# Kernel tuning notes

Measured on AMD Instinct MI355X. Metric: run time of the kernel, lower is better.

## Reference

```python
import jax, jax.numpy as jnp
import numpy as np


def setup_inputs() -> dict:
    key = jax.random.key(0)
    ks = jax.random.split(key, 8)
    B, C, W, H = 4, 256, 64, 64
    Cq = C // 8
    return {
        "input": jax.random.normal(ks[0], (B, C, W, H), dtype=jnp.float32),
        "Wf": jax.random.normal(ks[1], (Cq, C), dtype=jnp.float32) * 0.05,
        "bf": jax.random.normal(ks[2], (Cq,), dtype=jnp.float32) * 0.05,
        "Wg": jax.random.normal(ks[3], (Cq, C), dtype=jnp.float32) * 0.05,
        "bg": jax.random.normal(ks[4], (Cq,), dtype=jnp.float32) * 0.05,
        "Wh": jax.random.normal(ks[5], (C, C), dtype=jnp.float32) * 0.05,
        "bh": jax.random.normal(ks[6], (C,), dtype=jnp.float32) * 0.05,
        "gamma": jax.random.normal(ks[7], (1,), dtype=jnp.float32),
    }


def reference(input, Wf, bf, Wg, bg, Wh, bh, gamma):
    # input: [B, C, W, H]; SAGAN self-attention over N = W*H spatial tokens.
    B, C, W, H = input.shape
    N = W * H
    x = input.reshape(B, C, N)
    # 1x1 Conv1d == per-token linear projection over channels.
    f = jnp.einsum('oc,bcn->bon', Wf, x) + bf[None, :, None]  # [B, C/8, N]
    g = jnp.einsum('oc,bcn->bon', Wg, x) + bg[None, :, None]  # [B, C/8, N]
    h = jnp.einsum('oc,bcn->bon', Wh, x) + bh[None, :, None]  # [B, C,   N]
    # s = f^T g -> [B, N, N]; softmax over last dim (columns / g-tokens).
    s = jnp.einsum('bon,bom->bnm', f, g)
    attention = jax.nn.softmax(s, axis=-1)
    # out = h @ attention^T : out[b,c,m] = sum_n h[b,c,n] * attention[b,m,n]
    out = jnp.einsum('bcn,bmn->bcm', h, attention)
    out = out.reshape(B, C, W, H)
    return gamma[0] * out + input
```

## Files before the change

kernel.cpp:

```cpp
#include <hip/hip_runtime.h>

typedef _Float16 half8 __attribute__((ext_vector_type(8)));
typedef _Float16 half4 __attribute__((ext_vector_type(4)));
typedef unsigned int uintx2 __attribute__((ext_vector_type(2)));
typedef unsigned int uintx4 __attribute__((ext_vector_type(4)));
typedef float floatx16 __attribute__((ext_vector_type(16)));

#define MFMA_F16(A, B, C) __builtin_amdgcn_mfma_f32_32x32x16_f16(A, B, C, 0, 0, 0)

constexpr int Bn = 4;
constexpr int Cc = 256;
constexpr int Cq = 32;
constexpr int Nn = 4096;
constexpr float LOG2E = 1.44269504088896340736f;


__device__ inline floatx16 zero16() {
  floatx16 z;
#pragma unroll
  for (int i = 0; i < 16; ++i) z[i] = 0.f;
  return z;
}

__device__ inline unsigned int pkrtz(float a, float b) {
  return __builtin_bit_cast(unsigned int, __builtin_amdgcn_cvt_pkrtz(a, b));
}

__global__ __launch_bounds__(256) void k_wconv(
    const float* __restrict__ Wf, const float* __restrict__ Wg,
    const float* __restrict__ Wh, _Float16* __restrict__ Wfh,
    _Float16* __restrict__ Wgh, _Float16* __restrict__ Whh) {
  int e = (blockIdx.x * 256 + threadIdx.x) * 4;
  const float* src;
  _Float16* dst;
  float sc = 1.f;
  if (e < 8192) { src = Wf + e; dst = Wfh + e; sc = LOG2E; }
  else if (e < 16384) { src = Wg + (e - 8192); dst = Wgh + (e - 8192); }
  else { src = Wh + (e - 16384); dst = Whh + (e - 16384); }
  float4 v = *(const float4*)src;
  half4 o;
  o[0] = (_Float16)(v.x * sc); o[1] = (_Float16)(v.y * sc);
  o[2] = (_Float16)(v.z * sc); o[3] = (_Float16)(v.w * sc);
  *(half4*)dst = o;
}

__global__ __launch_bounds__(512) void k_qkv(
    const float* __restrict__ x,
    const _Float16* __restrict__ Wfh, const float* __restrict__ bf,
    const _Float16* __restrict__ Wgh, const float* __restrict__ bg,
    _Float16* __restrict__ Q, _Float16* __restrict__ K4,
    _Float16* __restrict__ V8) {
  __shared__ float xs[32][260];
  int tid = threadIdx.x;
  int w = tid >> 6, lane = tid & 63;
  int ml = lane & 31, h = lane >> 5;
  int b = blockIdx.x >> 7, nt = blockIdx.x & 127;
  int n0 = nt * 32;

  {
    int c = tid >> 3;
    int nl = (tid & 7) * 4;
    const float* xp = x + (size_t)b * Cc * Nn + n0 + nl;
#pragma unroll
    for (int pass = 0; pass < 4; ++pass) {
      int cc = c + pass * 64;
      float4 v = *(const float4*)(xp + (size_t)cc * Nn);
      xs[nl + 0][cc] = v.x;
      xs[nl + 1][cc] = v.y;
      xs[nl + 2][cc] = v.z;
      xs[nl + 3][cc] = v.w;
    }
  }
  __syncthreads();

  if (w < 2) {
    half8 bfr[16];
#pragma unroll
    for (int kc = 0; kc < 16; ++kc) {
      const float* xp = &xs[ml][kc * 16 + h * 8];
      half8 f;
#pragma unroll
      for (int j = 0; j < 8; ++j) f[j] = (_Float16)xp[j];
      bfr[kc] = f;
    }

    const _Float16* W = (w == 0) ? Wfh : Wgh;
    const float* bias = (w == 0) ? bf : bg;
    float bscale = (w == 0) ? LOG2E : 1.f;

    floatx16 acc = zero16();
    const _Float16* wp = W + (size_t)ml * Cc + h * 8;
#pragma unroll
    for (int kc = 0; kc < 16; ++kc) {
      half8 a = *(const half8*)(wp + kc * 16);
      acc = MFMA_F16(a, bfr[kc], acc);
    }

    if (w == 0) {
      _Float16* op = Q + ((size_t)b * Nn + n0 + ml) * Cq;
#pragma unroll
      for (int qd = 0; qd < 4; ++qd) {
        float4 bq = *(const float4*)(bias + 8 * qd + 4 * h);
        const float* bqp = (const float*)&bq;
#pragma unroll
        for (int i = 0; i < 4; ++i) {
          int crow = i + 8 * qd + 4 * h;
          op[crow] = (_Float16)(acc[4 * qd + i] + bqp[i] * bscale);
        }
      }
    } else {
#pragma unroll
      for (int qd = 0; qd < 4; ++qd) {
        float4 bq = *(const float4*)(bias + 8 * qd + 4 * h);
        const float* bqp = (const float*)&bq;
#pragma unroll
        for (int i = 0; i < 4; ++i) {
          int crow = i + 8 * qd + 4 * h;
          K4[(((size_t)b * 4 + (crow >> 3)) * Nn + n0 + ml) * 8 + (crow & 7)] =
              (_Float16)(acc[4 * qd + i] + bqp[i]);
        }
      }
    }
  }

#pragma unroll
  for (int gi = 0; gi < 2; ++gi) {
    int gidx = tid + gi * 512;
    int nbl = gidx >> 8, c = gidx & 255;
    half8 vv;
#pragma unroll
    for (int i = 0; i < 8; ++i) vv[i] = (_Float16)xs[nbl * 8 + i][c];
    *(half8*)(V8 + (((size_t)b * 512 + (n0 >> 3) + nbl) * 256 + c) * 8) = vv;
  }
}

__global__ __launch_bounds__(512) void k_rowmax(const _Float16* __restrict__ Q,
                                                const _Float16* __restrict__ K4,
                                                float* __restrict__ M) {
  __shared__ float red[8][32];
  int tid = threadIdx.x, w = tid >> 6, lane = tid & 63;
  int ml = lane & 31, h = lane >> 5;
  int b = blockIdx.x >> 7, mt = blockIdx.x & 127;
  int m0 = mt * 32;
  const _Float16* qp = Q + ((size_t)b * Nn + m0 + ml) * Cq + h * 8;
  half8 qb0 = *(const half8*)(qp);
  half8 qb1 = *(const half8*)(qp + 16);
  const _Float16* kp0 = K4 + (((size_t)b * 4 + h) * Nn + w * 512 + ml) * 8;
  const _Float16* kp1 = K4 + (((size_t)b * 4 + 2 + h) * Nn + w * 512 + ml) * 8;
  float mx = -3.0e38f;
  for (int t = 0; t < 16; ++t) {
    floatx16 s = zero16();
    half8 k0 = *(const half8*)(kp0 + (size_t)t * 32 * 8);
    half8 k1 = *(const half8*)(kp1 + (size_t)t * 32 * 8);
    s = MFMA_F16(k0, qb0, s);
    s = MFMA_F16(k1, qb1, s);
#pragma unroll
    for (int i = 0; i < 16; ++i) mx = fmaxf(mx, s[i]);
  }
  mx = fmaxf(mx, __shfl_xor(mx, 32, 64));
  if (h == 0) red[w][ml] = mx;
  __syncthreads();
  if (tid < 32) {
    float m2 = red[0][tid];
#pragma unroll
    for (int i = 1; i < 8; ++i) m2 = fmaxf(m2, red[i][tid]);
    M[(size_t)b * Nn + m0 + tid] = m2;
  }
}

__device__ inline void otree_write(float2* dst, const floatx16* o) {
#pragma unroll
  for (int cb = 0; cb < 8; ++cb)
#pragma unroll
    for (int rp = 0; rp < 8; ++rp)
      dst[(cb * 8 + rp) * 64] = make_float2(o[cb][2 * rp], o[cb][2 * rp + 1]);
}

__device__ inline void otree_add(const float2* src, floatx16* o) {
#pragma unroll
  for (int cb = 0; cb < 8; ++cb)
#pragma unroll
    for (int rp = 0; rp < 8; ++rp) {
      float2 v = src[(cb * 8 + rp) * 64];
      o[cb][2 * rp] += v.x;
      o[cb][2 * rp + 1] += v.y;
    }
}

__global__ __launch_bounds__(512, 2) void k_attn(
    const _Float16* __restrict__ Q, const _Float16* __restrict__ K4,
    const _Float16* __restrict__ V8, const float* __restrict__ M,
    const _Float16* __restrict__ Whh, const float* __restrict__ bh,
    const float* __restrict__ xin, const float* __restrict__ gamma,
    float* __restrict__ out) {
  __shared__ float Ored[4 * 8192];
  __shared__ float lred[8][32];
  int tid = threadIdx.x, w = tid >> 6, lane = tid & 63;
  int ml = lane & 31, h = lane >> 5;
  int mh = w >> 2, nw = w & 3;
  int bx = blockIdx.x;
  int mt = bx & 63, b = bx >> 6;
  int mb = mt * 64;
  int m0 = mb + mh * 32;

  const _Float16* qp = Q + ((size_t)b * Nn + m0 + ml) * Cq + h * 8;
  half8 qb0 = *(const half8*)(qp);
  half8 qb1 = *(const half8*)(qp + 16);
  float Mv = M[(size_t)b * Nn + m0 + ml];
  float g = gamma[0];
  float lacc = 0.f;

  const _Float16* k4b0 = K4 + (((size_t)b * 4 + h) * Nn + nw * 32 + ml) * 8;
  const _Float16* k4b1 = K4 + (((size_t)b * 4 + 2 + h) * Nn + nw * 32 + ml) * 8;
  const _Float16* v8b = V8 + (((size_t)b * 512 + nw * 4 + h) * 256 + ml) * 8;

  floatx16 o[8];
#pragma unroll
  for (int i = 0; i < 8; ++i) o[i] = zero16();

  half8 k0 = *(const half8*)(k4b0);
  half8 k1 = *(const half8*)(k4b1);

  for (int it = 0; it < 32; ++it) {
    floatx16 s = zero16();
    s = MFMA_F16(k0, qb0, s);
    s = MFMA_F16(k1, qb1, s);
    k0 = *(const half8*)(k4b0 + (size_t)(it + 1) * 1024);
    k1 = *(const half8*)(k4b1 + (size_t)(it + 1) * 1024);
    float p[16];
#pragma unroll
    for (int i = 0; i < 16; ++i) p[i] = __builtin_amdgcn_exp2f(s[i] - Mv);
#pragma unroll
    for (int i = 0; i < 16; ++i) lacc += p[i];
    unsigned int c0 = pkrtz(p[0], p[1]),  c1 = pkrtz(p[2], p[3]);
    unsigned int c2 = pkrtz(p[4], p[5]),  c3 = pkrtz(p[6], p[7]);
    unsigned int c4 = pkrtz(p[8], p[9]),  c5 = pkrtz(p[10], p[11]);
    unsigned int c6 = pkrtz(p[12], p[13]), c7 = pkrtz(p[14], p[15]);
    uintx2 t02 = __builtin_amdgcn_permlane32_swap(c0, c2, false, false);
    uintx2 t13 = __builtin_amdgcn_permlane32_swap(c1, c3, false, false);
    uintx2 t46 = __builtin_amdgcn_permlane32_swap(c4, c6, false, false);
    uintx2 t57 = __builtin_amdgcn_permlane32_swap(c5, c7, false, false);
    uintx4 f0v = {t02.x, t13.x, t02.y, t13.y};
    uintx4 f1v = {t46.x, t57.x, t46.y, t57.y};
    half8 pf0 = __builtin_bit_cast(half8, f0v);
    half8 pf1 = __builtin_bit_cast(half8, f1v);
    const _Float16* vp = v8b + (size_t)it * 32768;
#pragma unroll
    for (int cb = 0; cb < 8; ++cb) {
      half8 vf0 = *(const half8*)(vp + cb * 256);
      o[cb] = MFMA_F16(vf0, pf0, o[cb]);
    }
#pragma unroll
    for (int cb = 0; cb < 8; ++cb) {
      half8 vf1 = *(const half8*)(vp + 4096 + cb * 256);
      o[cb] = MFMA_F16(vf1, pf1, o[cb]);
    }
  }

  lacc += __shfl_xor(lacc, 32, 64);
  if (h == 0) lred[w][ml] = lacc;

  float2* Ored2 = (float2*)Ored;
  int lofs = h * 32 + ml;
  float2* rg0 = Ored2 + (size_t)(mh * 2) * 4096 + lofs;
  float2* rg1 = Ored2 + (size_t)(mh * 2 + 1) * 4096 + lofs;
  if (nw == 2) otree_write(rg0, o);
  if (nw == 3) otree_write(rg1, o);
  __syncthreads();
  if (nw == 0) otree_add(rg0, o);
  if (nw == 1) otree_add(rg1, o);
  __syncthreads();
  if (nw == 1) otree_write(rg1, o);
  __syncthreads();
  if (nw == 0) { otree_add(rg1, o); otree_write(rg0, o); }
  __syncthreads();

  float lv0 = lred[0][ml] + lred[1][ml] + lred[2][ml] + lred[3][ml];
  float lv1 = lred[4][ml] + lred[5][ml] + lred[6][ml] + lred[7][ml];
  float il0 = g / lv0;
  float il1 = g / lv1;
  int offs[8];
#pragma unroll
  for (int j = 0; j < 8; ++j) {
    int u = h * 8 + j;
    int rb = (u & 3) | ((u >> 3) << 2);
    int hw = (u >> 2) & 1;
    offs[j] = (rb >> 1) * 128 + hw * 64 + 2 * ml + (rb & 1);
  }
  const float* R0 = Ored;
  const float* R1 = Ored + 2 * 8192;
  int c0 = w * 32;
  const _Float16* whp = Whh + (size_t)(c0 + ml) * 256 + h * 8;
  floatx16 d0 = zero16(), d1 = zero16();
#pragma unroll
  for (int kq = 0; kq < 16; ++kq) {
    half8 a = *(const half8*)(whp + kq * 16);
    float q0[8], q1[8];
#pragma unroll
    for (int j = 0; j < 8; ++j) {
      q0[j] = R0[kq * 512 + offs[j]] * il0;
      q1[j] = R1[kq * 512 + offs[j]] * il1;
    }
    uintx4 b0v = {pkrtz(q0[0], q0[1]), pkrtz(q0[2], q0[3]),
                  pkrtz(q0[4], q0[5]), pkrtz(q0[6], q0[7])};
    uintx4 b1v = {pkrtz(q1[0], q1[1]), pkrtz(q1[2], q1[3]),
                  pkrtz(q1[4], q1[5]), pkrtz(q1[6], q1[7])};
    d0 = MFMA_F16(a, __builtin_bit_cast(half8, b0v), d0);
    d1 = MFMA_F16(a, __builtin_bit_cast(half8, b1v), d1);
  }

  size_t ob = (size_t)b * 256 * (size_t)Nn;
#pragma unroll
  for (int r = 0; r < 16; ++r) {
    int c = c0 + (r & 3) + 8 * (r >> 2) + 4 * h;
    float bias = g * bh[c];
    size_t oa0 = ob + (size_t)c * Nn + mb + ml;
    size_t oa1 = oa0 + 32;
    out[oa0] = d0[r] + bias + xin[oa0];
    out[oa1] = d1[r] + bias + xin[oa1];
  }
}

extern "C" void kernel_launch(void* const* d_in, const int* in_sizes, int n_in,
                              void* d_out, int out_size, void* d_ws,
                              size_t ws_size, hipStream_t stream) {
  const float* x = (const float*)d_in[0];
  const float* Wf = (const float*)d_in[1];
  const float* bf = (const float*)d_in[2];
  const float* Wg = (const float*)d_in[3];
  const float* bg = (const float*)d_in[4];
  const float* Wh = (const float*)d_in[5];
  const float* bh = (const float*)d_in[6];
  const float* gamma = (const float*)d_in[7];
  float* out = (float*)d_out;

  char* ws = (char*)d_ws;
  _Float16* Q  = (_Float16*)(ws);
  _Float16* K4 = (_Float16*)(ws + 1048576);
  _Float16* V8 = (_Float16*)(ws + 2097152);
  float*    M  = (float*)   (ws + 10485760);
  _Float16* Wfh = (_Float16*)(ws + 10551296);
  _Float16* Wgh = (_Float16*)(ws + 10567680);
  _Float16* Whh = (_Float16*)(ws + 10584064);

  k_wconv<<<dim3(80), dim3(256), 0, stream>>>(Wf, Wg, Wh, Wfh, Wgh, Whh);
  k_qkv<<<dim3(512), dim3(512), 0, stream>>>(x, Wfh, bf, Wgh, bg, Q, K4, V8);
  k_rowmax<<<dim3(512), dim3(512), 0, stream>>>(Q, K4, M);
  k_attn<<<dim3(256), dim3(512), 0, stream>>>(Q, K4, V8, M, Whh, bh, x, gamma, out);
}
```

Measured before the change: 151.6 us.

## Double-buffer V tiles in LDS via async global_load_lds in attention loop

Stages each 64KB V chunk into shared memory with direct global-to-LDS loads, double-buffered so the next chunk loads while the current one feeds the MFMAs. The shared buffer is reused afterwards for the output reduction. The aim is to hide global latency for V reads and to share one copy of V across the waves in a block. The cost is a block-wide barrier with full vmcnt/lgkmcnt waits every iteration, and 128KB of LDS that likely cuts occupancy from 2 blocks per CU to 1.

```diff
diff --git a/kernel.cpp b/kernel.cpp
--- a/kernel.cpp
+++ b/kernel.cpp
@@ -24,6 +24,20 @@
 
 __device__ inline unsigned int pkrtz(float a, float b) {
   return __builtin_bit_cast(unsigned int, __builtin_amdgcn_cvt_pkrtz(a, b));
+}
+
+__device__ inline void stage64k(const _Float16* __restrict__ src,
+                                _Float16* dst, int w, int lane) {
+  const char* gb = (const char*)src;
+  char* lb = (char*)dst;
+#pragma unroll
+  for (int i = 0; i < 8; ++i) {
+    int off = (w * 8 + i) * 1024;
+    __builtin_amdgcn_global_load_lds(
+        (const __attribute__((address_space(1))) unsigned int*)(gb + off + lane * 16),
+        (__attribute__((address_space(3))) unsigned int*)(lb + off),
+        16, 0, 0);
+  }
 }
 
 __global__ __launch_bounds__(256) void k_wconv(
@@ -193,8 +207,12 @@
     const _Float16* __restrict__ Whh, const float* __restrict__ bh,
     const float* __restrict__ xin, const float* __restrict__ gamma,
     float* __restrict__ out) {
-  __shared__ float Ored[4 * 8192];
+  __shared__ __align__(16) char smem[131072];
   __shared__ float lred[8][32];
+  _Float16* vbuf = (_Float16*)smem;
+  float* OredF = (float*)smem;
+  float2* Ored2 = (float2*)smem;
+
   int tid = threadIdx.x, w = tid >> 6, lane = tid & 63;
   int ml = lane & 31, h = lane >> 5;
   int mh = w >> 2, nw = w & 3;
@@ -212,21 +230,31 @@
 
   const _Float16* k4b0 = K4 + (((size_t)b * 4 + h) * Nn + nw * 32 + ml) * 8;
   const _Float16* k4b1 = K4 + (((size_t)b * 4 + 2 + h) * Nn + nw * 32 + ml) * 8;
-  const _Float16* v8b = V8 + (((size_t)b * 512 + nw * 4 + h) * 256 + ml) * 8;
+  const _Float16* vchunk = V8 + (size_t)b * 512 * 2048;
 
   floatx16 o[8];
 #pragma unroll
   for (int i = 0; i < 8; ++i) o[i] = zero16();
 
+  stage64k(vchunk, vbuf, w, lane);
   half8 k0 = *(const half8*)(k4b0);
   half8 k1 = *(const half8*)(k4b1);
+  asm volatile("s_waitcnt vmcnt(0)" ::: "memory");
+  __builtin_amdgcn_s_barrier();
+  __builtin_amdgcn_sched_barrier(0);
+
+  const _Float16* vrd = vbuf + ((nw * 4 + h) * 2048 + ml * 8);
+  int cur = 0;
 
   for (int it = 0; it < 32; ++it) {
+    if (it < 31)
+      stage64k(vchunk + (size_t)(it + 1) * 32768, vbuf + (cur ^ 1) * 32768, w, lane);
+    half8 kn0 = *(const half8*)(k4b0 + (size_t)(it + 1) * 1024);
+    half8 kn1 = *(const half8*)(k4b1 + (size_t)(it + 1) * 1024);
+
     floatx16 s = zero16();
     s = MFMA_F16(k0, qb0, s);
     s = MFMA_F16(k1, qb1, s);
-    k0 = *(const half8*)(k4b0 + (size_t)(it + 1) * 1024);
-    k1 = *(const half8*)(k4b1 + (size_t)(it + 1) * 1024);
     float p[16];
 #pragma unroll
     for (int i = 0; i < 16; ++i) p[i] = __builtin_amdgcn_exp2f(s[i] - Mv);
@@ -244,7 +272,8 @@
     uintx4 f1v = {t46.x, t57.x, t46.y, t57.y};
     half8 pf0 = __builtin_bit_cast(half8, f0v);
     half8 pf1 = __builtin_bit_cast(half8, f1v);
-    const _Float16* vp = v8b + (size_t)it * 32768;
+
+    const _Float16* vp = vrd + cur * 32768;
 #pragma unroll
     for (int cb = 0; cb < 8; ++cb) {
       half8 vf0 = *(const half8*)(vp + cb * 256);
@@ -255,12 +284,18 @@
       half8 vf1 = *(const half8*)(vp + 4096 + cb * 256);
       o[cb] = MFMA_F16(vf1, pf1, o[cb]);
     }
+
+    asm volatile("s_waitcnt lgkmcnt(0)" ::: "memory");
+    asm volatile("s_waitcnt vmcnt(0)" ::: "memory");
+    __builtin_amdgcn_s_barrier();
+    __builtin_amdgcn_sched_barrier(0);
+    cur ^= 1;
+    k0 = kn0; k1 = kn1;
   }
 
   lacc += __shfl_xor(lacc, 32, 64);
   if (h == 0) lred[w][ml] = lacc;
 
-  float2* Ored2 = (float2*)Ored;
   int lofs = h * 32 + ml;
   float2* rg0 = Ored2 + (size_t)(mh * 2) * 4096 + lofs;
   float2* rg1 = Ored2 + (size_t)(mh * 2 + 1) * 4096 + lofs;
@@ -287,10 +322,10 @@
     int hw = (u >> 2) & 1;
     offs[j] = (rb >> 1) * 128 + hw * 64 + 2 * ml + (rb & 1);
   }
-  const float* R0 = Ored;
-  const float* R1 = Ored + 2 * 8192;
-  int c0 = w * 32;
-  const _Float16* whp = Whh + (size_t)(c0 + ml) * 256 + h * 8;
+  const float* R0 = OredF;
+  const float* R1 = OredF + 2 * 8192;
+  int c0w = w * 32;
+  const _Float16* whp = Whh + (size_t)(c0w + ml) * 256 + h * 8;
   floatx16 d0 = zero16(), d1 = zero16();
 #pragma unroll
   for (int kq = 0; kq < 16; ++kq) {
@@ -312,7 +347,7 @@
   size_t ob = (size_t)b * 256 * (size_t)Nn;
 #pragma unroll
   for (int r = 0; r < 16; ++r) {
-    int c = c0 + (r & 3) + 8 * (r >> 2) + 4 * h;
+    int c = c0w + (r & 3) + 8 * (r >> 2) + 4 * h;
     float bias = g * bh[c];
     size_t oa0 = ob + (size_t)c * Nn + mb + ml;
     size_t oa1 = oa0 + 32;
```

After: 152.2 us. No clear change (+0.4%).
